# Kernel optimization log

Measured on AMD Instinct MI355X. Metric: run time of the kernel, lower is better.

## Reference

```python
import jax, jax.numpy as jnp
import numpy as np

NUM_HEADS = 8
ALPHA = 4.0
BN_EPS = 1e-5


def _dwconv(x, w, pad):
    # x: [B, C, H, W], w: [C, 1, kh, kw] depthwise (groups == C)
    return jax.lax.conv_general_dilated(
        x, w, window_strides=(1, 1), padding=[(pad, pad), (pad, pad)],
        dimension_numbers=('NCHW', 'OIHW', 'NCHW'),
        feature_group_count=x.shape[1])


def _forward(x, qg_w, kv_w, proj_w, proj_b, dwc_w, dwc_b, power_p, scale_p,
             enh_w, bn_gamma, bn_beta, enhance_weight, pos_enc):
    B, N, C = x.shape
    H = W = int(round(N ** 0.5))
    h = NUM_HEADS
    d = C // h

    # qg linear (no bias): [B, N, 2C] -> q, g
    qg = jnp.einsum('bnc,oc->bno', x, qg_w)
    q, g = qg[..., :C], qg[..., C:]

    # SpatialFilterEnhancer on q: depthwise 3x3 conv + BN(train) + ReLU
    qi = q.transpose(0, 2, 1).reshape(B, C, H, W)
    qe = _dwconv(qi, enh_w, pad=1)
    m = qe.mean(axis=(0, 2, 3), keepdims=True)
    var = qe.var(axis=(0, 2, 3), keepdims=True)
    qe = (qe - m) * jax.lax.rsqrt(var + BN_EPS)
    qe = qe * bn_gamma[None, :, None, None] + bn_beta[None, :, None, None]
    qe = jax.nn.relu(qe)
    q_enh = qe.reshape(B, C, N).transpose(0, 2, 1)
    q = q + enhance_weight * q_enh

    # kv linear (sr_ratio == 1 path)
    kv = jnp.einsum('bnc,oc->bno', x, kv_w)
    k, v = kv[..., :C], kv[..., C:]
    k = k + pos_enc  # learned positional encoding, shape [1, N, C]
    n = k.shape[1]

    scale = jax.nn.softplus(scale_p)              # [1, 1, C]
    power = 1.0 + ALPHA * jax.nn.sigmoid(power_p)  # [1, h, 1, d]
    q = q / scale
    k = k / scale

    # split heads: [B, h, N, d]
    q = q.reshape(B, N, h, d).transpose(0, 2, 1, 3)
    k = k.reshape(B, n, h, d).transpose(0, 2, 1, 3)
    v = v.reshape(B, n, h, d).transpose(0, 2, 1, 3)

    # power-law kernel feature maps
    q_pos = jax.nn.relu(q) ** power
    q_neg = jax.nn.relu(-q) ** power
    k_pos = jax.nn.relu(k) ** power
    k_neg = jax.nn.relu(-k) ** power
    q_sim = jnp.concatenate([q_pos, q_neg], axis=-1)   # [B, h, N, 2d]
    q_opp = jnp.concatenate([q_neg, q_pos], axis=-1)
    kf = jnp.concatenate([k_pos, k_neg], axis=-1)      # [B, h, n, 2d]
    v1, v2 = jnp.split(v, 2, axis=-1)                  # [B, h, n, d/2] each

    k_mean = kf.mean(axis=-2)  # [B, h, 2d]
    inv_n = 1.0 / n

    # sim branch
    z = 1.0 / (jnp.einsum('bhnd,bhd->bhn', q_sim, k_mean)[..., None] + 1e-6)
    kv1 = jnp.einsum('bhnd,bhne->bhde', kf, v1) * inv_n  # (n^-0.5)*(n^-0.5)
    x_sim = jnp.einsum('bhnd,bhde->bhne', q_sim, kv1) * z

    # opp branch
    z2 = 1.0 / (jnp.einsum('bhnd,bhd->bhn', q_opp, k_mean)[..., None] + 1e-6)
    kv2 = jnp.einsum('bhnd,bhne->bhde', kf, v2) * inv_n
    x_opp = jnp.einsum('bhnd,bhde->bhne', q_opp, kv2) * z2

    xa = jnp.concatenate([x_sim, x_opp], axis=-1)       # [B, h, N, d]
    xa = xa.transpose(0, 2, 1, 3).reshape(B, N, C)

    # depthwise conv positional branch on v (sr_ratio == 1 -> no interpolate)
    vimg = v.reshape(B * h, H, W, d).transpose(0, 3, 1, 2)  # [B*h, d, H, W]
    vd = _dwconv(vimg, dwc_w, pad=2) + dwc_b[None, :, None, None]
    v_out = vd.reshape(B, C, N).transpose(0, 2, 1)          # [B, N, C]

    out = (xa + v_out) * g
    out = jnp.einsum('bnc,oc->bno', out, proj_w) + proj_b
    return out


def setup_inputs() -> dict:
    key = jax.random.key(0)
    ks = jax.random.split(key, 10)
    B, N, C = 8, 3136, 512
    h = NUM_HEADS
    d = C // h
    f = lambda k, shape, s=0.02: jax.random.normal(k, shape, jnp.float32) * s
    return dict(
        x=jax.random.normal(ks[0], (B, N, C), jnp.float32),
        qg_w=f(ks[1], (2 * C, C)),
        kv_w=f(ks[2], (2 * C, C)),
        proj_w=f(ks[3], (C, C)),
        proj_b=jnp.zeros((C,), jnp.float32),
        dwc_w=f(ks[4], (d, 1, 5, 5), 0.1),
        dwc_b=jnp.zeros((d,), jnp.float32),
        power_p=f(ks[5], (1, h, 1, d), 0.1),
        scale_p=f(ks[6], (1, 1, C), 0.1),
        enh_w=f(ks[7], (C, 1, 3, 3), 0.1),
        bn_gamma=jnp.ones((C,), jnp.float32),
        bn_beta=jnp.zeros((C,), jnp.float32),
        enhance_weight=jnp.float32(0.5),
        pos_enc=f(ks[8], (1, N, C)),
    )


def reference(x, qg_w, kv_w, proj_w, proj_b, dwc_w, dwc_b, power_p, scale_p,
              enh_w, bn_gamma, bn_beta, enhance_weight, pos_enc):
    return _forward(x, qg_w, kv_w, proj_w, proj_b, dwc_w, dwc_b, power_p,
                    scale_p, enh_w, bn_gamma, bn_beta, enhance_weight, pos_enc)
```

## Files before the change

kernel.cpp:

```cpp
#include <hip/hip_runtime.h>
#include <hip/hip_bf16.h>
#include <math.h>

#define CDIM 512
#define NTOK 3136
#define BATCH 8
#define MTOT (BATCH*NTOK)
#define NHEAD 8
#define DHEAD 64
#define HW 56

typedef __attribute__((ext_vector_type(8))) short short8;
typedef __attribute__((ext_vector_type(4))) float f32x4;

__device__ __forceinline__ ushort f2bf(float f) {
    union { float f; unsigned int u; } v; v.f = f;
    unsigned int u = v.u + 0x7FFFu + ((v.u >> 16) & 1u);
    return (ushort)(u >> 16);
}
__device__ __forceinline__ float bf2f(ushort u) {
    union { unsigned int u; float f; } v; v.u = ((unsigned int)u) << 16;
    return v.f;
}

__device__ __forceinline__ void gload_lds16(const void* g, void* lds) {
    __builtin_amdgcn_global_load_lds((const __attribute__((address_space(1))) void*)g,
                                     (__attribute__((address_space(3))) void*)lds,
                                     16, 0, 0);
}

__global__ void prep_kernel(const float* __restrict__ scale_p,
                            const float* __restrict__ power_p,
                            float* __restrict__ inv_scale,
                            float* __restrict__ power) {
    int c = threadIdx.x;
    if (c < CDIM) {
        float s = log1pf(expf(scale_p[c]));
        inv_scale[c] = 1.0f / s;
        power[c] = 1.0f + 4.0f / (1.0f + expf(-power_p[c]));
    }
}

__global__ __launch_bounds__(256) void cvt_bf16_kernel(const float* __restrict__ src,
                                                       ushort* __restrict__ dst, int n4) {
    int i = blockIdx.x * 256 + threadIdx.x;
    if (i < n4) {
        float4 f = ((const float4*)src)[i];
        ushort4 o;
        o.x = f2bf(f.x); o.y = f2bf(f.y); o.z = f2bf(f.z); o.w = f2bf(f.w);
        ((ushort4*)dst)[i] = o;
    }
}

__global__ __launch_bounds__(256) void mgemm_qgkv(const ushort* __restrict__ A,
                                                  const ushort* __restrict__ Wqg,
                                                  const ushort* __restrict__ Wkv,
                                                  ushort* __restrict__ Qout,
                                                  ushort* __restrict__ Gout,
                                                  ushort* __restrict__ KFout,
                                                  ushort* __restrict__ Vout,
                                                  const float* __restrict__ pos,
                                                  const float* __restrict__ invs,
                                                  const float* __restrict__ powr) {
    __shared__ __align__(16) char smem[65536];
    ushort* At = (ushort*)smem;
    ushort* Bt = (ushort*)(smem + 32768);
    float*  Osh = (float*)smem;

    const int t = threadIdx.x;
    const int w = t >> 6, l = t & 63;
    const int wr = w >> 1, wc = w & 1;
    const int r8 = l >> 3, sl = l & 7;
    const int ss = sl ^ r8;

    const int bid = blockIdx.x;
    const int idp = (bid & 7) * 392 + (bid >> 3);
    const int mb = idp >> 4, ob = idp & 15;
    const int m0 = mb * 128;
    const ushort* Bp = (ob < 8) ? (Wqg + (size_t)ob * 128 * CDIM)
                                : (Wkv + (size_t)(ob - 8) * 128 * CDIM);

    auto stage = [&](int buf, int ks) {
        const int k0 = ks * 64;
        #pragma unroll
        for (int c = 0; c < 4; ++c) {
            int rc = (w * 4 + c) * 8 + r8;
            gload_lds16(A + (size_t)(m0 + rc) * CDIM + k0 + ss * 8, At + buf * 8192 + (w * 4 + c) * 512);
            gload_lds16(Bp + (size_t)rc * CDIM + k0 + ss * 8, Bt + buf * 8192 + (w * 4 + c) * 512);
        }
    };

    f32x4 acc[4][4] = {};
    stage(0, 0);
    __syncthreads();
    for (int ks = 0; ks < 8; ++ks) {
        int cur = ks & 1;
        if (ks < 7) stage(cur ^ 1, ks + 1);
        #pragma unroll
        for (int kk = 0; kk < 2; ++kk) {
            short8 af[4], bfr[4];
            const int sbase = kk * 4 + (l >> 4);
            #pragma unroll
            for (int i = 0; i < 4; ++i) {
                int row = wr * 64 + i * 16 + (l & 15);
                af[i] = *(const short8*)&At[cur * 8192 + row * 64 + ((sbase ^ (row & 7)) * 8)];
                int rowb = wc * 64 + i * 16 + (l & 15);
                bfr[i] = *(const short8*)&Bt[cur * 8192 + rowb * 64 + ((sbase ^ (rowb & 7)) * 8)];
            }
            #pragma unroll
            for (int i = 0; i < 4; ++i)
                #pragma unroll
                for (int j = 0; j < 4; ++j)
                    acc[i][j] = __builtin_amdgcn_mfma_f32_16x16x32_bf16(af[i], bfr[j], acc[i][j], 0, 0, 0);
        }
        __syncthreads();
    }

    #pragma unroll
    for (int i = 0; i < 4; ++i)
        #pragma unroll
        for (int j = 0; j < 4; ++j)
            #pragma unroll
            for (int rr = 0; rr < 4; ++rr) {
                int row = wr * 64 + i * 16 + (l >> 4) * 4 + rr;
                int col = wc * 64 + j * 16 + (l & 15);
                int pc = col ^ (((row >> 2) & 1) << 4);
                Osh[row * 128 + pc] = acc[i][j][rr];
            }
    __syncthreads();

    const int colbase = ob * 128;
    #pragma unroll
    for (int q = 0; q < 16; ++q) {
        int fi = q * 256 + t;
        int r = fi >> 5, c4 = (fi & 31) * 4;
        int pc4 = c4 ^ (((r >> 2) & 1) << 4);
        float4 v = *(float4*)&Osh[r * 128 + pc4];
        int m = m0 + r;
        if (colbase < 512) {
            ushort4 o;
            o.x = f2bf(v.x); o.y = f2bf(v.y); o.z = f2bf(v.z); o.w = f2bf(v.w);
            *(ushort4*)&Qout[(size_t)m * CDIM + colbase + c4] = o;
        } else if (colbase < 1024) {
            ushort4 o;
            o.x = f2bf(v.x); o.y = f2bf(v.y); o.z = f2bf(v.z); o.w = f2bf(v.w);
            *(ushort4*)&Gout[(size_t)m * CDIM + colbase - 512 + c4] = o;
        } else if (colbase < 1536) {
            int n = m % NTOK;
            int oc = colbase - 1024 + c4;
            float4 pv = *(const float4*)&pos[(size_t)n * CDIM + oc];
            float4 iv = *(const float4*)&invs[oc];
            float4 pw = *(const float4*)&powr[oc];
            float kx0 = (v.x + pv.x) * iv.x, kx1 = (v.y + pv.y) * iv.y;
            float kx2 = (v.z + pv.z) * iv.z, kx3 = (v.w + pv.w) * iv.w;
            float t0 = __powf(fabsf(kx0), pw.x), t1 = __powf(fabsf(kx1), pw.y);
            float t2 = __powf(fabsf(kx2), pw.z), t3 = __powf(fabsf(kx3), pw.w);
            ushort4 up, un;
            up.x = kx0 > 0.f ? f2bf(t0) : 0; un.x = kx0 < 0.f ? f2bf(t0) : 0;
            up.y = kx1 > 0.f ? f2bf(t1) : 0; un.y = kx1 < 0.f ? f2bf(t1) : 0;
            up.z = kx2 > 0.f ? f2bf(t2) : 0; un.z = kx2 < 0.f ? f2bf(t2) : 0;
            up.w = kx3 > 0.f ? f2bf(t3) : 0; un.w = kx3 < 0.f ? f2bf(t3) : 0;
            ushort* dst = KFout + (size_t)m * 1024 + ((oc >> 6) << 7) + (oc & 63);
            *(ushort4*)dst = up;
            *(ushort4*)(dst + 64) = un;
        } else {
            ushort4 o;
            o.x = f2bf(v.x); o.y = f2bf(v.y); o.z = f2bf(v.z); o.w = f2bf(v.w);
            *(ushort4*)&Vout[(size_t)m * CDIM + colbase - 1536 + c4] = o;
        }
    }
}

__global__ __launch_bounds__(256) void mgemm_proj(const ushort* __restrict__ A,
                                                  const ushort* __restrict__ W,
                                                  float* __restrict__ out,
                                                  const float* __restrict__ pb) {
    __shared__ __align__(16) char smem[65536];
    ushort* At = (ushort*)smem;
    ushort* Bt = (ushort*)(smem + 32768);
    float*  Osh = (float*)smem;

    const int t = threadIdx.x;
    const int w = t >> 6, l = t & 63;
    const int wr = w >> 1, wc = w & 1;
    const int r8 = l >> 3, sl = l & 7;
    const int ss = sl ^ r8;

    const int bid = blockIdx.x;
    const int idp = (bid & 7) * 98 + (bid >> 3);
    const int mb = idp >> 2, ob = idp & 3;
    const int m0 = mb * 128;
    const ushort* Bp = W + (size_t)ob * 128 * CDIM;

    auto stage = [&](int buf, int ks) {
        const int k0 = ks * 64;
        #pragma unroll
        for (int c = 0; c < 4; ++c) {
            int rc = (w * 4 + c) * 8 + r8;
            gload_lds16(A + (size_t)(m0 + rc) * CDIM + k0 + ss * 8, At + buf * 8192 + (w * 4 + c) * 512);
            gload_lds16(Bp + (size_t)rc * CDIM + k0 + ss * 8, Bt + buf * 8192 + (w * 4 + c) * 512);
        }
    };

    f32x4 acc[4][4] = {};
    stage(0, 0);
    __syncthreads();
    for (int ks = 0; ks < 8; ++ks) {
        int cur = ks & 1;
        if (ks < 7) stage(cur ^ 1, ks + 1);
        #pragma unroll
        for (int kk = 0; kk < 2; ++kk) {
            short8 af[4], bfr[4];
            const int sbase = kk * 4 + (l >> 4);
            #pragma unroll
            for (int i = 0; i < 4; ++i) {
                int row = wr * 64 + i * 16 + (l & 15);
                af[i] = *(const short8*)&At[cur * 8192 + row * 64 + ((sbase ^ (row & 7)) * 8)];
                int rowb = wc * 64 + i * 16 + (l & 15);
                bfr[i] = *(const short8*)&Bt[cur * 8192 + rowb * 64 + ((sbase ^ (rowb & 7)) * 8)];
            }
            #pragma unroll
            for (int i = 0; i < 4; ++i)
                #pragma unroll
                for (int j = 0; j < 4; ++j)
                    acc[i][j] = __builtin_amdgcn_mfma_f32_16x16x32_bf16(af[i], bfr[j], acc[i][j], 0, 0, 0);
        }
        __syncthreads();
    }

    #pragma unroll
    for (int i = 0; i < 4; ++i)
        #pragma unroll
        for (int j = 0; j < 4; ++j)
            #pragma unroll
            for (int rr = 0; rr < 4; ++rr) {
                int row = wr * 64 + i * 16 + (l >> 4) * 4 + rr;
                int col = wc * 64 + j * 16 + (l & 15);
                int pc = col ^ (((row >> 2) & 1) << 4);
                Osh[row * 128 + pc] = acc[i][j][rr];
            }
    __syncthreads();

    const int colbase = ob * 128;
    #pragma unroll
    for (int q = 0; q < 16; ++q) {
        int fi = q * 256 + t;
        int r = fi >> 5, c4 = (fi & 31) * 4;
        int pc4 = c4 ^ (((r >> 2) & 1) << 4);
        float4 v = *(float4*)&Osh[r * 128 + pc4];
        float4 b4 = *(const float4*)&pb[colbase + c4];
        v.x += b4.x; v.y += b4.y; v.z += b4.z; v.w += b4.w;
        *(float4*)&out[(size_t)(m0 + r) * CDIM + colbase + c4] = v;
    }
}

__global__ __launch_bounds__(256) void conv3s_kernel(const ushort* __restrict__ Qbf,
                                                     const float* __restrict__ enh_w,
                                                     ushort* __restrict__ QEbf,
                                                     float* __restrict__ ssum,
                                                     float* __restrict__ ssq) {
    const int t = threadIdx.x;
    const int c0 = t * 2;
    const int xpos = blockIdx.x;
    const int byc = blockIdx.y;
    const int b = byc >> 2, yc = byc & 3;
    const int y0 = yc * 14;

    float wgt[9][2];
    #pragma unroll
    for (int tap = 0; tap < 9; ++tap) {
        wgt[tap][0] = enh_w[c0 * 9 + tap];
        wgt[tap][1] = enh_w[(c0 + 1) * 9 + tap];
    }
    const size_t base = (size_t)b * NTOK * CDIM + c0;

    float2 win[3][3];
    auto ldrow = [&](int yy, float2* dst) {
        #pragma unroll
        for (int dx = 0; dx < 3; ++dx) {
            int xx = xpos + dx - 1;
            bool ok = (yy >= 0 && yy < HW && xx >= 0 && xx < HW);
            if (ok) {
                ushort2 uv = *(const ushort2*)(Qbf + base + ((size_t)(yy * HW + xx) << 9));
                dst[dx] = make_float2(bf2f(uv.x), bf2f(uv.y));
            } else {
                dst[dx] = make_float2(0.f, 0.f);
            }
        }
    };
    ldrow(y0 - 1, win[0]);
    ldrow(y0,     win[1]);

    float s1a = 0.f, s2a = 0.f, s1b = 0.f, s2b = 0.f;
    #pragma unroll
    for (int i = 0; i < 14; ++i) {
        int y = y0 + i;
        ldrow(y + 1, win[(i + 2) % 3]);
        float a0 = 0.f, a1 = 0.f;
        #pragma unroll
        for (int dy = 0; dy < 3; ++dy) {
            float2* row = win[(i + dy) % 3];
            #pragma unroll
            for (int dx = 0; dx < 3; ++dx) {
                a0 = fmaf(row[dx].x, wgt[dy * 3 + dx][0], a0);
                a1 = fmaf(row[dx].y, wgt[dy * 3 + dx][1], a1);
            }
        }
        ushort2 o; o.x = f2bf(a0); o.y = f2bf(a1);
        *(ushort2*)(QEbf + base + ((size_t)(y * HW + xpos) << 9)) = o;
        s1a += a0; s2a += a0 * a0;
        s1b += a1; s2b += a1 * a1;
    }
    atomicAdd(&ssum[c0], s1a);     atomicAdd(&ssq[c0], s2a);
    atomicAdd(&ssum[c0 + 1], s1b); atomicAdd(&ssq[c0 + 1], s2b);
}

__global__ void bnprep_kernel(const float* __restrict__ ssum, const float* __restrict__ ssq,
                              const float* __restrict__ bn_g, const float* __restrict__ bn_b,
                              float* __restrict__ achan, float* __restrict__ bchan) {
    int c = threadIdx.x;
    if (c < CDIM) {
        const float invM = 1.0f / (float)MTOT;
        float mean = ssum[c] * invM;
        float var  = ssq[c] * invM - mean * mean;
        float a = bn_g[c] * rsqrtf(var + 1e-5f);
        achan[c] = a;
        bchan[c] = bn_b[c] - mean * a;
    }
}

__global__ __launch_bounds__(256) void kvred4_kernel(const ushort* __restrict__ KF,
                                                     const ushort* __restrict__ Vbf,
                                                     float* __restrict__ PKV) {
    const int bh = blockIdx.x, chunk = blockIdx.y;
    const int b = bh >> 3, head = bh & 7;
    const int t = threadIdx.x;
    const int w = t >> 6, l = t & 63;
    const int lr = l & 15;
    const int ns = (l >> 4) * 8;

    const int nbase = b * NTOK + chunk * 448;
    const ushort* kf0 = KF  + ((size_t)(nbase + ns)) * 1024 + head * 128 + (w * 32 + lr);
    const ushort* vb0 = Vbf + ((size_t)(nbase + ns)) * 512  + head * 64  + lr;

    short8 ones;
    #pragma unroll
    for (int j = 0; j < 8; ++j) ones[j] = (lr == 0) ? (short)0x3F80 : (short)0;

    f32x4 acc[2][5] = {};
    for (int tile = 0; tile < 14; ++tile) {
        union { uint u[4]; short8 s; } ua[2], ub[4];
        #pragma unroll
        for (int i = 0; i < 2; ++i) {
            #pragma unroll
            for (int j = 0; j < 4; ++j) {
                uint lo = kf0[i * 16 + (size_t)(2 * j) * 1024];
                uint hi = kf0[i * 16 + (size_t)(2 * j + 1) * 1024];
                ua[i].u[j] = lo | (hi << 16);
            }
        }
        #pragma unroll
        for (int j5 = 0; j5 < 4; ++j5) {
            #pragma unroll
            for (int j = 0; j < 4; ++j) {
                uint lo = vb0[j5 * 16 + (size_t)(2 * j) * 512];
                uint hi = vb0[j5 * 16 + (size_t)(2 * j + 1) * 512];
                ub[j5].u[j] = lo | (hi << 16);
            }
        }
        #pragma unroll
        for (int i = 0; i < 2; ++i) {
            #pragma unroll
            for (int j5 = 0; j5 < 4; ++j5)
                acc[i][j5] = __builtin_amdgcn_mfma_f32_16x16x32_bf16(ua[i].s, ub[j5].s, acc[i][j5], 0, 0, 0);
            acc[i][4] = __builtin_amdgcn_mfma_f32_16x16x32_bf16(ua[i].s, ones, acc[i][4], 0, 0, 0);
        }
        kf0 += (size_t)32 * 1024;
        vb0 += (size_t)32 * 512;
    }
    size_t base = ((size_t)(chunk * 64 + bh)) * 8320;
    #pragma unroll
    for (int i = 0; i < 2; ++i) {
        int d0 = w * 32 + i * 16 + (l >> 4) * 4;
        #pragma unroll
        for (int j = 0; j < 5; ++j) {
            int e = j * 16 + lr;
            if (j < 4 || e == 64)
                *(f32x4*)(PKV + base + (size_t)e * 128 + d0) = acc[i][j];
        }
    }
}

__global__ __launch_bounds__(256) void kvreduce2_kernel(const float* __restrict__ PKV,
                                                        ushort* __restrict__ kvTbf) {
    int gid = blockIdx.x * 256 + threadIdx.x;
    const float inv_n = 1.0f / (float)NTOK;
    int bh = gid / 10240;
    int r  = gid - bh * 10240;
    int row = r >> 7, dcol = r & 127;
    int dlog = (((dcol >> 3) ^ (row & 7)) << 3) | (dcol & 7);
    float s = 0.f;
    if (row < 64) {
        int dsel = (row >= 32) ? (dlog ^ 64) : dlog;
        #pragma unroll
        for (int c = 0; c < 7; ++c) s += PKV[(size_t)c * 532480 + (size_t)bh * 8320 + row * 128 + dsel];
    } else if (row < 66) {
        int dsel = (row == 65) ? (dlog ^ 64) : dlog;
        #pragma unroll
        for (int c = 0; c < 7; ++c) s += PKV[(size_t)c * 532480 + (size_t)bh * 8320 + 64 * 128 + dsel];
    }
    kvTbf[gid] = (row < 66) ? f2bf(s * inv_n) : (ushort)0;
}

__global__ __launch_bounds__(256) void attn_mfma_kernel(const ushort* __restrict__ Qbf,
                                                        const ushort* __restrict__ QEbf,
                                                        const ushort* __restrict__ kvTbf,
                                                        const float* __restrict__ power,
                                                        const float* __restrict__ achan,
                                                        const float* __restrict__ bchan,
                                                        const float* __restrict__ invs,
                                                        const float* __restrict__ ewp,
                                                        ushort* __restrict__ ATTbf) {
    __shared__ ushort QF[64 * 128];
    __shared__ ushort BT[80 * 128];
    const int bh = blockIdx.x, tb = blockIdx.y;
    const int b = bh >> 3, head = bh & 7;
    const int t = threadIdx.x;
    const int w = t >> 6, l = t & 63;

    #pragma unroll
    for (int i = 0; i < 5; ++i) {
        int f = i * 256 + t;
        gload_lds16(kvTbf + (size_t)bh * 10240 + f * 8, BT + f * 8);
    }

    const int c = l, hc = head * 64 + c;
    const float p = power[hc];
    const float ac = achan[hc], bc = bchan[hc], iv = invs[hc], ew = ewp[0];
    #pragma unroll
    for (int i = 0; i < 16; ++i) {
        int tok = i * 4 + w;
        size_t off = ((size_t)(b * NTOK + tb * 64 + tok)) * CDIM + hc;
        float q = bf2f(Qbf[off]);
        float qe = bf2f(QEbf[off]);
        q = (q + ew * fmaxf(fmaf(ac, qe, bc), 0.f)) * iv;
        float ax = fabsf(q);
        float tp = ax > 0.f ? __powf(ax, p) : 0.f;
        float qp = q > 0.f ? tp : 0.f;
        float qn = q < 0.f ? tp : 0.f;
        int sw = tok & 7;
        QF[tok * 128 + (((c >> 3) ^ sw) * 8) + (c & 7)]       = f2bf(qp);
        QF[tok * 128 + ((((c >> 3) + 8) ^ sw) * 8) + (c & 7)] = f2bf(qn);
    }
    __syncthreads();

    f32x4 acc[5] = {};
    #pragma unroll
    for (int kk = 0; kk < 4; ++kk) {
        int sbase = kk * 4 + (l >> 4);
        int rowa = w * 16 + (l & 15);
        short8 af = *(const short8*)&QF[rowa * 128 + ((sbase ^ (rowa & 7)) * 8)];
        #pragma unroll
        for (int j = 0; j < 5; ++j) {
            int rowb = j * 16 + (l & 15);
            short8 bf = *(const short8*)&BT[rowb * 128 + ((sbase ^ (rowb & 7)) * 8)];
            acc[j] = __builtin_amdgcn_mfma_f32_16x16x32_bf16(af, bf, acc[j], 0, 0, 0);
        }
    }
    __syncthreads();

    ushort* Oout = QF;
    #pragma unroll
    for (int rr = 0; rr < 4; ++rr) {
        float ssim = __shfl(acc[4][rr], (l & 48));
        float sopp = __shfl(acc[4][rr], (l & 48) + 1);
        float zs = 1.f / (ssim + 1e-6f);
        float zo = 1.f / (sopp + 1e-6f);
        int tokl = w * 16 + (l >> 4) * 4 + rr;
        #pragma unroll
        for (int j = 0; j < 4; ++j) {
            int e = j * 16 + (l & 15);
            Oout[tokl * 64 + e] = f2bf(acc[j][rr] * (j < 2 ? zs : zo));
        }
    }
    __syncthreads();

    #pragma unroll
    for (int i = 0; i < 2; ++i) {
        int idx = i * 256 + t;
        int tokl = idx >> 3, ch = (idx & 7) * 8;
        short8 vv = *(short8*)&Oout[tokl * 64 + ch];
        *(short8*)&ATTbf[((size_t)(b * NTOK + tb * 64 + tokl)) * CDIM + head * 64 + ch] = vv;
    }
}

__global__ __launch_bounds__(256) void voutg2_kernel(const ushort* __restrict__ Vbf,
                                                     const ushort* __restrict__ ATTbf,
                                                     const ushort* __restrict__ Gbf,
                                                     const float* __restrict__ dwc_w,
                                                     const float* __restrict__ dwc_b,
                                                     ushort* __restrict__ PRE) {
    const int t = threadIdx.x;
    const int c0 = t * 2;
    const int xpos = blockIdx.x;
    const int byc = blockIdx.y;
    const int b = byc >> 2, yc = byc & 3;
    const int y0 = yc * 14;
    const int dch = c0 & 63;

    float wgt[25][2];
    #pragma unroll
    for (int tap = 0; tap < 25; ++tap) {
        wgt[tap][0] = dwc_w[dch * 25 + tap];
        wgt[tap][1] = dwc_w[(dch + 1) * 25 + tap];
    }
    const float bias0 = dwc_b[dch], bias1 = dwc_b[dch + 1];
    const size_t base = (size_t)b * NTOK * CDIM + c0;

    float2 win[5][5];
    auto ldrow = [&](int yy, float2* dst) {
        #pragma unroll
        for (int dx = 0; dx < 5; ++dx) {
            int xx = xpos + dx - 2;
            bool ok = (yy >= 0 && yy < HW && xx >= 0 && xx < HW);
            if (ok) {
                ushort2 uv = *(const ushort2*)(Vbf + base + ((size_t)(yy * HW + xx) << 9));
                dst[dx] = make_float2(bf2f(uv.x), bf2f(uv.y));
            } else {
                dst[dx] = make_float2(0.f, 0.f);
            }
        }
    };
    ldrow(y0 - 2, win[0]);
    ldrow(y0 - 1, win[1]);
    ldrow(y0,     win[2]);
    ldrow(y0 + 1, win[3]);

    #pragma unroll
    for (int i = 0; i < 14; ++i) {
        int y = y0 + i;
        ldrow(y + 2, win[(i + 4) % 5]);
        float a0 = bias0, a1 = bias1;
        #pragma unroll
        for (int dy = 0; dy < 5; ++dy) {
            float2* row = win[(i + dy) % 5];
            #pragma unroll
            for (int dx = 0; dx < 5; ++dx) {
                a0 = fmaf(row[dx].x, wgt[dy * 5 + dx][0], a0);
                a1 = fmaf(row[dx].y, wgt[dy * 5 + dx][1], a1);
            }
        }
        size_t oidx = base + ((size_t)(y * HW + xpos) << 9);
        ushort2 au = *(const ushort2*)(ATTbf + oidx);
        ushort2 gu = *(const ushort2*)(Gbf + oidx);
        ushort2 o;
        o.x = f2bf((bf2f(au.x) + a0) * bf2f(gu.x));
        o.y = f2bf((bf2f(au.y) + a1) * bf2f(gu.y));
        *(ushort2*)(PRE + oidx) = o;
    }
}

extern "C" void kernel_launch(void* const* d_in, const int* in_sizes, int n_in,
                              void* d_out, int out_size, void* d_ws, size_t ws_size,
                              hipStream_t stream) {
    const float* x      = (const float*)d_in[0];
    const float* qg_w   = (const float*)d_in[1];
    const float* kv_w   = (const float*)d_in[2];
    const float* proj_w = (const float*)d_in[3];
    const float* proj_b = (const float*)d_in[4];
    const float* dwc_w  = (const float*)d_in[5];
    const float* dwc_b  = (const float*)d_in[6];
    const float* power_p= (const float*)d_in[7];
    const float* scale_p= (const float*)d_in[8];
    const float* enh_w  = (const float*)d_in[9];
    const float* bn_g   = (const float*)d_in[10];
    const float* bn_b   = (const float*)d_in[11];
    const float* ew_p   = (const float*)d_in[12];
    const float* pos    = (const float*)d_in[13];

    const size_t NELEM = (size_t)MTOT * CDIM;
    float* ws    = (float*)d_ws;
    ushort* Qbf  = (ushort*)ws;
    ushort* Gbf  = (ushort*)(ws + NELEM);
    float*  PKV  = ws + NELEM + NELEM / 2;
    ushort* KFbf = (ushort*)(ws + 2 * NELEM);
    ushort* PREbf= (ushort*)(ws + 2 * NELEM);
    ushort* Vbf  = (ushort*)(ws + 3 * NELEM);
    ushort* ATTbf= (ushort*)(ws + 3 * NELEM + NELEM / 2);
    ushort* Xbf  = (ushort*)(ws + 4 * NELEM);
    ushort* QEbf = (ushort*)(ws + 4 * NELEM);
    float* SMALL = ws + 5 * NELEM;
    float* ssum  = SMALL;
    float* ssq   = SMALL + 512;
    ushort* kvTbf= (ushort*)(SMALL + 9216);
    float* invs  = SMALL + 533504;
    float* powr  = SMALL + 534016;
    float* achan = SMALL + 534528;
    float* bchan = SMALL + 535040;
    ushort* Wqg  = (ushort*)(SMALL + 535552);
    ushort* Wkv  = (ushort*)(SMALL + 797696);
    ushort* Wproj= (ushort*)(SMALL + 1059840);

    hipMemsetAsync(SMALL, 0, (size_t)1024 * sizeof(float), stream);

    prep_kernel<<<1, 512, 0, stream>>>(scale_p, power_p, invs, powr);

    cvt_bf16_kernel<<<12544, 256, 0, stream>>>(x, Xbf, 3211264);
    cvt_bf16_kernel<<<512, 256, 0, stream>>>(qg_w, Wqg, 131072);
    cvt_bf16_kernel<<<512, 256, 0, stream>>>(kv_w, Wkv, 131072);
    cvt_bf16_kernel<<<256, 256, 0, stream>>>(proj_w, Wproj, 65536);

    mgemm_qgkv<<<3136, 256, 0, stream>>>(Xbf, Wqg, Wkv, Qbf, Gbf, KFbf, Vbf, pos, invs, powr);

    dim3 cgrid(56, 32);
    conv3s_kernel<<<cgrid, 256, 0, stream>>>(Qbf, enh_w, QEbf, ssum, ssq);
    bnprep_kernel<<<1, 512, 0, stream>>>(ssum, ssq, bn_g, bn_b, achan, bchan);

    kvred4_kernel<<<dim3(64, 7), 256, 0, stream>>>(KFbf, Vbf, PKV);
    kvreduce2_kernel<<<2560, 256, 0, stream>>>(PKV, kvTbf);

    attn_mfma_kernel<<<dim3(64, 49), 256, 0, stream>>>(Qbf, QEbf, kvTbf, powr,
                                                       achan, bchan, invs, ew_p, ATTbf);

    voutg2_kernel<<<cgrid, 256, 0, stream>>>(Vbf, ATTbf, Gbf, dwc_w, dwc_b, PREbf);

    mgemm_proj<<<784, 256, 0, stream>>>(PREbf, Wproj, (float*)d_out, proj_b);
}
```

Measured before the change: 502.2 us.

## Keep Q in fp32, merge weight conversions, split KV reduction finer

Three separate changes. Q from the QG/KV GEMM is now stored as fp32 instead of bf16 and read as fp32 by the conv and attention kernels, which doubles Q memory traffic but removes one rounding step. The three weight bf16 conversions are merged into one launch to cut launch overhead. The KV partial reduction now uses 14 chunks instead of 7, spread over two workspace buffers, to raise parallelism at the price of a larger final reduce.

```diff
diff --git a/kernel.cpp b/kernel.cpp
--- a/kernel.cpp
+++ b/kernel.cpp
@@ -52,10 +52,27 @@
     }
 }
 
+__global__ __launch_bounds__(256) void cvt_weights_kernel(const float* __restrict__ qg_w,
+                                                          const float* __restrict__ kv_w,
+                                                          const float* __restrict__ proj_w,
+                                                          ushort* __restrict__ Wqg,
+                                                          ushort* __restrict__ Wkv,
+                                                          ushort* __restrict__ Wproj) {
+    int i = blockIdx.x * 256 + threadIdx.x;
+    const float* src; ushort* dst; int idx;
+    if (i < 131072)      { src = qg_w;   dst = Wqg;   idx = i; }
+    else if (i < 262144) { src = kv_w;   dst = Wkv;   idx = i - 131072; }
+    else                 { src = proj_w; dst = Wproj; idx = i - 262144; }
+    float4 f = ((const float4*)src)[idx];
+    ushort4 o;
+    o.x = f2bf(f.x); o.y = f2bf(f.y); o.z = f2bf(f.z); o.w = f2bf(f.w);
+    ((ushort4*)dst)[idx] = o;
+}
+
 __global__ __launch_bounds__(256) void mgemm_qgkv(const ushort* __restrict__ A,
                                                   const ushort* __restrict__ Wqg,
                                                   const ushort* __restrict__ Wkv,
-                                                  ushort* __restrict__ Qout,
+                                                  float* __restrict__ Qout,
                                                   ushort* __restrict__ Gout,
                                                   ushort* __restrict__ KFout,
                                                   ushort* __restrict__ Vout,
@@ -138,9 +155,7 @@
         float4 v = *(float4*)&Osh[r * 128 + pc4];
         int m = m0 + r;
         if (colbase < 512) {
-            ushort4 o;
-            o.x = f2bf(v.x); o.y = f2bf(v.y); o.z = f2bf(v.z); o.w = f2bf(v.w);
-            *(ushort4*)&Qout[(size_t)m * CDIM + colbase + c4] = o;
+            *(float4*)&Qout[(size_t)m * CDIM + colbase + c4] = v;
         } else if (colbase < 1024) {
             ushort4 o;
             o.x = f2bf(v.x); o.y = f2bf(v.y); o.z = f2bf(v.z); o.w = f2bf(v.w);
@@ -254,7 +269,7 @@
     }
 }
 
-__global__ __launch_bounds__(256) void conv3s_kernel(const ushort* __restrict__ Qbf,
+__global__ __launch_bounds__(256) void conv3s_kernel(const float* __restrict__ Q,
                                                      const float* __restrict__ enh_w,
                                                      ushort* __restrict__ QEbf,
                                                      float* __restrict__ ssum,
@@ -280,12 +295,8 @@
         for (int dx = 0; dx < 3; ++dx) {
             int xx = xpos + dx - 1;
             bool ok = (yy >= 0 && yy < HW && xx >= 0 && xx < HW);
-            if (ok) {
-                ushort2 uv = *(const ushort2*)(Qbf + base + ((size_t)(yy * HW + xx) << 9));
-                dst[dx] = make_float2(bf2f(uv.x), bf2f(uv.y));
-            } else {
-                dst[dx] = make_float2(0.f, 0.f);
-            }
+            dst[dx] = ok ? *(const float2*)(Q + base + ((size_t)(yy * HW + xx) << 9))
+                         : make_float2(0.f, 0.f);
         }
     };
     ldrow(y0 - 1, win[0]);
@@ -331,7 +342,8 @@
 
 __global__ __launch_bounds__(256) void kvred4_kernel(const ushort* __restrict__ KF,
                                                      const ushort* __restrict__ Vbf,
-                                                     float* __restrict__ PKV) {
+                                                     float* __restrict__ PKV_A,
+                                                     float* __restrict__ PKV_B) {
     const int bh = blockIdx.x, chunk = blockIdx.y;
     const int b = bh >> 3, head = bh & 7;
     const int t = threadIdx.x;
@@ -339,7 +351,7 @@
     const int lr = l & 15;
     const int ns = (l >> 4) * 8;
 
-    const int nbase = b * NTOK + chunk * 448;
+    const int nbase = b * NTOK + chunk * 224;
     const ushort* kf0 = KF  + ((size_t)(nbase + ns)) * 1024 + head * 128 + (w * 32 + lr);
     const ushort* vb0 = Vbf + ((size_t)(nbase + ns)) * 512  + head * 64  + lr;
 
@@ -348,7 +360,7 @@
     for (int j = 0; j < 8; ++j) ones[j] = (lr == 0) ? (short)0x3F80 : (short)0;
 
     f32x4 acc[2][5] = {};
-    for (int tile = 0; tile < 14; ++tile) {
+    for (int tile = 0; tile < 7; ++tile) {
         union { uint u[4]; short8 s; } ua[2], ub[4];
         #pragma unroll
         for (int i = 0; i < 2; ++i) {
@@ -378,7 +390,9 @@
         kf0 += (size_t)32 * 1024;
         vb0 += (size_t)32 * 512;
     }
-    size_t base = ((size_t)(chunk * 64 + bh)) * 8320;
+    float* dstb = (chunk < 7)
+        ? (PKV_A + ((size_t)(chunk * 64 + bh)) * 8320)
+        : (PKV_B + ((size_t)((chunk - 7) * 64 + bh)) * 8320);
     #pragma unroll
     for (int i = 0; i < 2; ++i) {
         int d0 = w * 32 + i * 16 + (l >> 4) * 4;
@@ -386,12 +400,13 @@
         for (int j = 0; j < 5; ++j) {
             int e = j * 16 + lr;
             if (j < 4 || e == 64)
-                *(f32x4*)(PKV + base + (size_t)e * 128 + d0) = acc[i][j];
-        }
-    }
-}
-
-__global__ __launch_bounds__(256) void kvreduce2_kernel(const float* __restrict__ PKV,
+                *(f32x4*)(dstb + (size_t)e * 128 + d0) = acc[i][j];
+        }
+    }
+}
+
+__global__ __launch_bounds__(256) void kvreduce2_kernel(const float* __restrict__ PKV_A,
+                                                        const float* __restrict__ PKV_B,
                                                         ushort* __restrict__ kvTbf) {
     int gid = blockIdx.x * 256 + threadIdx.x;
     const float inv_n = 1.0f / (float)NTOK;
@@ -400,19 +415,20 @@
     int row = r >> 7, dcol = r & 127;
     int dlog = (((dcol >> 3) ^ (row & 7)) << 3) | (dcol & 7);
     float s = 0.f;
-    if (row < 64) {
-        int dsel = (row >= 32) ? (dlog ^ 64) : dlog;
-        #pragma unroll
-        for (int c = 0; c < 7; ++c) s += PKV[(size_t)c * 532480 + (size_t)bh * 8320 + row * 128 + dsel];
-    } else if (row < 66) {
-        int dsel = (row == 65) ? (dlog ^ 64) : dlog;
-        #pragma unroll
-        for (int c = 0; c < 7; ++c) s += PKV[(size_t)c * 532480 + (size_t)bh * 8320 + 64 * 128 + dsel];
+    if (row < 66) {
+        int rsel, dsel;
+        if (row < 64) { rsel = row; dsel = (row >= 32) ? (dlog ^ 64) : dlog; }
+        else          { rsel = 64;  dsel = (row == 65) ? (dlog ^ 64) : dlog; }
+        size_t idx = (size_t)bh * 8320 + rsel * 128 + dsel;
+        #pragma unroll
+        for (int c = 0; c < 7; ++c) s += PKV_A[(size_t)c * 532480 + idx];
+        #pragma unroll
+        for (int c = 0; c < 7; ++c) s += PKV_B[(size_t)c * 532480 + idx];
     }
     kvTbf[gid] = (row < 66) ? f2bf(s * inv_n) : (ushort)0;
 }
 
-__global__ __launch_bounds__(256) void attn_mfma_kernel(const ushort* __restrict__ Qbf,
+__global__ __launch_bounds__(256) void attn_mfma_kernel(const float* __restrict__ Q,
                                                         const ushort* __restrict__ QEbf,
                                                         const ushort* __restrict__ kvTbf,
                                                         const float* __restrict__ power,
@@ -441,7 +457,7 @@
     for (int i = 0; i < 16; ++i) {
         int tok = i * 4 + w;
         size_t off = ((size_t)(b * NTOK + tb * 64 + tok)) * CDIM + hc;
-        float q = bf2f(Qbf[off]);
+        float q = Q[off];
         float qe = bf2f(QEbf[off]);
         q = (q + ew * fmaxf(fmaf(ac, qe, bc), 0.f)) * iv;
         float ax = fabsf(q);
@@ -580,15 +596,16 @@
 
     const size_t NELEM = (size_t)MTOT * CDIM;
     float* ws    = (float*)d_ws;
-    ushort* Qbf  = (ushort*)ws;
+    float*  Qf   = ws;
     ushort* Gbf  = (ushort*)(ws + NELEM);
-    float*  PKV  = ws + NELEM + NELEM / 2;
+    float*  PKV_A= ws + NELEM + NELEM / 2;
     ushort* KFbf = (ushort*)(ws + 2 * NELEM);
     ushort* PREbf= (ushort*)(ws + 2 * NELEM);
     ushort* Vbf  = (ushort*)(ws + 3 * NELEM);
     ushort* ATTbf= (ushort*)(ws + 3 * NELEM + NELEM / 2);
     ushort* Xbf  = (ushort*)(ws + 4 * NELEM);
     ushort* QEbf = (ushort*)(ws + 4 * NELEM);
+    float*  PKV_B= ws + 4 * NELEM + NELEM / 2;
     float* SMALL = ws + 5 * NELEM;
     float* ssum  = SMALL;
     float* ssq   = SMALL + 512;
@@ -606,20 +623,18 @@
     prep_kernel<<<1, 512, 0, stream>>>(scale_p, power_p, invs, powr);
 
     cvt_bf16_kernel<<<12544, 256, 0, stream>>>(x, Xbf, 3211264);
-    cvt_bf16_kernel<<<512, 256, 0, stream>>>(qg_w, Wqg, 131072);
-    cvt_bf16_kernel<<<512, 256, 0, stream>>>(kv_w, Wkv, 131072);
-    cvt_bf16_kernel<<<256, 256, 0, stream>>>(proj_w, Wproj, 65536);
-
-    mgemm_qgkv<<<3136, 256, 0, stream>>>(Xbf, Wqg, Wkv, Qbf, Gbf, KFbf, Vbf, pos, invs, powr);
+    cvt_weights_kernel<<<1280, 256, 0, stream>>>(qg_w, kv_w, proj_w, Wqg, Wkv, Wproj);
+
+    mgemm_qgkv<<<3136, 256, 0, stream>>>(Xbf, Wqg, Wkv, Qf, Gbf, KFbf, Vbf, pos, invs, powr);
 
     dim3 cgrid(56, 32);
-    conv3s_kernel<<<cgrid, 256, 0, stream>>>(Qbf, enh_w, QEbf, ssum, ssq);
+    conv3s_kernel<<<cgrid, 256, 0, stream>>>(Qf, enh_w, QEbf, ssum, ssq);
     bnprep_kernel<<<1, 512, 0, stream>>>(ssum, ssq, bn_g, bn_b, achan, bchan);
 
-    kvred4_kernel<<<dim3(64, 7), 256, 0, stream>>>(KFbf, Vbf, PKV);
-    kvreduce2_kernel<<<2560, 256, 0, stream>>>(PKV, kvTbf);
-
-    attn_mfma_kernel<<<dim3(64, 49), 256, 0, stream>>>(Qbf, QEbf, kvTbf, powr,
+    kvred4_kernel<<<dim3(64, 14), 256, 0, stream>>>(KFbf, Vbf, PKV_A, PKV_B);
+    kvreduce2_kernel<<<2560, 256, 0, stream>>>(PKV_A, PKV_B, kvTbf);
+
+    attn_mfma_kernel<<<dim3(64, 49), 256, 0, stream>>>(Qf, QEbf, kvTbf, powr,
                                                        achan, bchan, invs, ew_p, ATTbf);
 
     voutg2_kernel<<<cgrid, 256, 0, stream>>>(Vbf, ATTbf, Gbf, dwc_w, dwc_b, PREbf);
```

Result: faster. 481.9 us (-4.0%).
